# Kernel tuning notes

Measured on AMD Instinct MI355X. Metric: run time of the kernel, lower is better.

The kernel has to match this reference:

```python
import jax, jax.numpy as jnp
import numpy as np

N = 50000   # nodes
E = 800000  # edges (avg degree 16)
D = 128     # node latent dim
DE = 128    # edge latent dim
L = 3       # num_mp_steps


def setup_inputs() -> dict:
    key = jax.random.key(0)
    ks = jax.random.split(key, 10)
    s = 0.05
    return dict(
        x=jax.random.normal(ks[0], (N, D), jnp.float32),
        edge_index=jax.random.randint(ks[1], (2, E), 0, N, jnp.int32),
        edge_attr=jax.random.normal(ks[2], (E, DE), jnp.float32),
        # per-layer GATConv params (stacked over L layers)
        W=jax.random.normal(ks[3], (L, D, D), jnp.float32) * s,        # lin (shared src/dst)
        att_src=jax.random.normal(ks[4], (L, D), jnp.float32) * s,
        att_dst=jax.random.normal(ks[5], (L, D), jnp.float32) * s,
        W_e=jax.random.normal(ks[6], (L, DE, D), jnp.float32) * s,     # lin_edge
        att_edge=jax.random.normal(ks[7], (L, D), jnp.float32) * s,
        bias=jnp.zeros((L, D), jnp.float32),
        ln_gamma=jnp.ones((L, D), jnp.float32),                        # post-conv LayerNorm
        ln_beta=jnp.zeros((L, D), jnp.float32),
    )


def reference(x, edge_index, edge_attr, W, att_src, att_dst, W_e, att_edge, bias, ln_gamma, ln_beta):
    n = x.shape[0]
    src, dst = edge_index[0], edge_index[1]

    # add_self_loops with fill_value='mean': self-loop edge feature of node i is
    # the mean of raw edge features of edges incoming to i (0 if none).
    ones = jnp.ones((src.shape[0],), x.dtype)
    deg = jax.ops.segment_sum(ones, dst, num_segments=n)
    loop_attr = jax.ops.segment_sum(edge_attr, dst, num_segments=n) / jnp.maximum(deg, 1.0)[:, None]
    loop = jnp.arange(n, dtype=src.dtype)
    src_f = jnp.concatenate([src, loop])            # [E+N]
    dst_f = jnp.concatenate([dst, loop])            # [E+N]
    ea_f = jnp.concatenate([edge_attr, loop_attr], axis=0)  # [E+N, DE]

    def layer(h_in, p):
        Wl, asl, adl, Wel, ael, bl, gl, bel = p
        h = h_in @ Wl                                              # [N, D]
        # per-edge attention logits (heads=1)
        a = (h @ asl)[src_f] + (h @ adl)[dst_f] + ea_f @ (Wel @ ael)  # [E+N]
        a = jnp.where(a > 0, a, 0.2 * a)                           # LeakyReLU(0.2)
        # segment softmax over destination nodes (every node has a self loop)
        m = jax.ops.segment_max(a, dst_f, num_segments=n)
        ea = jnp.exp(a - m[dst_f])
        denom = jax.ops.segment_sum(ea, dst_f, num_segments=n)
        alpha = ea / denom[dst_f]
        out = jax.ops.segment_sum(h[src_f] * alpha[:, None], dst_f, num_segments=n) + bl
        # LayerNorm (elementwise affine)
        mu = jnp.mean(out, axis=-1, keepdims=True)
        var = jnp.var(out, axis=-1, keepdims=True)
        out = (out - mu) * jax.lax.rsqrt(var + 1e-5) * gl + bel
        return out, None

    h, _ = jax.lax.scan(layer, x, (W, att_src, att_dst, W_e, att_edge, bias, ln_gamma, ln_beta))
    return h
```

## Files before the change

kernel.cpp:

```cpp
#include <hip/hip_runtime.h>
#include <cstdint>

#define D 128
#define LNUM 3

typedef short short8 __attribute__((ext_vector_type(8)));
typedef float f32x4 __attribute__((ext_vector_type(4)));
typedef float f32x2 __attribute__((ext_vector_type(2)));

static __device__ __forceinline__ float wred_sum(float x) {
#pragma unroll
    for (int off = 32; off; off >>= 1) x += __shfl_xor(x, off);
    return x;
}
static __device__ __forceinline__ float wred_max(float x) {
#pragma unroll
    for (int off = 32; off; off >>= 1) x = fmaxf(x, __shfl_xor(x, off));
    return x;
}
static __device__ __forceinline__ uint32_t f2bf_rne(float x) {
    uint32_t u = __float_as_uint(x);
    uint32_t r = u + 0x7fffu + ((u >> 16) & 1u);
    return r >> 16;
}


__global__ __launch_bounds__(256) void pre_k(const float* __restrict__ W, const float* __restrict__ We,
                                             const float* __restrict__ ae, const float* __restrict__ x,
                                             const int* __restrict__ dst,
                                             uint16_t* __restrict__ Wt, float* __restrict__ vbuf,
                                             uint16_t* __restrict__ xb, int* __restrict__ cnt,
                                             int ND4, int E) {
    int tid = blockIdx.x * 256 + threadIdx.x;
    int stride = gridDim.x * 256;
    for (int i = tid; i < ND4; i += stride) {
        float4 v = *(const float4*)&x[(size_t)i * 4];
        uint2 o;
        o.x = f2bf_rne(v.x) | (f2bf_rne(v.y) << 16);
        o.y = f2bf_rne(v.z) | (f2bf_rne(v.w) << 16);
        *(uint2*)&xb[(size_t)i * 4] = o;
    }
    for (int e = tid; e < E; e += stride) atomicAdd(&cnt[dst[e]], 1);
    for (int i = tid; i < LNUM * D * D; i += stride) {
        int l = i >> 14;
        int r = i & (D * D - 1);
        int j = r >> 7, k = r & 127;
        Wt[i] = (uint16_t)f2bf_rne(W[(size_t)l * D * D + (size_t)k * D + j]);
    }
    if (tid < LNUM * D) {
        int l = tid >> 7, j = tid & 127;
        const float* Wrow = We + ((size_t)l * D + j) * D;
        const float* a = ae + (size_t)l * D;
        float s = 0.f;
        for (int d = 0; d < D; ++d) s += Wrow[d] * a[d];
        vbuf[tid] = s;
    }
}


__global__ __launch_bounds__(1024) void scan_k(const int* __restrict__ cnt, int* __restrict__ rowptr, int N) {
    __shared__ int sh[1024];
    int t = threadIdx.x;
    int chunk = (N + 1023) >> 10;
    int b = t * chunk;
    int e = min(b + chunk, N);
    int s = 0;
    for (int i = b; i < e; ++i) s += cnt[i];
    sh[t] = s;
    __syncthreads();
    for (int off = 1; off < 1024; off <<= 1) {
        int v = (t >= off) ? sh[t - off] : 0;
        __syncthreads();
        sh[t] += v;
        __syncthreads();
    }
    int run = sh[t] - s;
    for (int i = b; i < e; ++i) { rowptr[i] = run; run += cnt[i]; }
    if (t == 1023) rowptr[N] = sh[1023];
}


static __device__ __forceinline__ void gemm_body(uint4* As, int bid, int t,
                                                 const uint16_t* __restrict__ A,
                                                 const uint16_t* __restrict__ Wt,
                                                 const float* __restrict__ as_,
                                                 const float* __restrict__ ad_,
                                                 uint16_t* __restrict__ hbf,
                                                 float* __restrict__ hs, float* __restrict__ hd, int N) {
    int row0 = bid * 64;
#pragma unroll
    for (int it = 0; it < 4; ++it) {
        int idx2 = it * 256 + t;
        int r = idx2 >> 4, s = idx2 & 15;
        int gr = row0 + r;
        uint4 v = make_uint4(0u, 0u, 0u, 0u);
        if (gr < N) v = *(const uint4*)&A[(size_t)gr * D + s * 8];
        As[r * 16 + (s ^ (r & 7))] = v;
    }
    __syncthreads();
    int w = t >> 6, l = t & 63;
    int lrow = l & 15, lk = l >> 4;
    int rbase = w * 16;
    short8 afrag[4];
#pragma unroll
    for (int ks = 0; ks < 4; ++ks) {
        int r = rbase + lrow;
        int s = (ks * 4 + lk) ^ (r & 7);
        afrag[ks] = __builtin_bit_cast(short8, As[r * 16 + s]);
    }
    float psum[4] = {0.f, 0.f, 0.f, 0.f}, pdum[4] = {0.f, 0.f, 0.f, 0.f};
#pragma unroll
    for (int ct = 0; ct < 8; ++ct) {
        f32x4 acc = {0.f, 0.f, 0.f, 0.f};
#pragma unroll
        for (int ks = 0; ks < 4; ++ks) {
            short8 b = *(const short8*)&Wt[(size_t)(ct * 16 + lrow) * D + ks * 32 + lk * 8];
            acc = __builtin_amdgcn_mfma_f32_16x16x32_bf16(afrag[ks], b, acc, 0, 0, 0);
        }
        int col_g = ct * 16 + lrow;
        float av = as_[col_g], dv = ad_[col_g];
#pragma unroll
        for (int r = 0; r < 4; ++r) {
            float v = acc[r];
            psum[r] += v * av;
            pdum[r] += v * dv;
            int row_g = row0 + rbase + lk * 4 + r;
            if (row_g < N) hbf[(size_t)row_g * D + col_g] = (uint16_t)f2bf_rne(v);
        }
    }
#pragma unroll
    for (int r = 0; r < 4; ++r) {
        float ps = psum[r], pd = pdum[r];
#pragma unroll
        for (int off = 1; off < 16; off <<= 1) {
            ps += __shfl_xor(ps, off);
            pd += __shfl_xor(pd, off);
        }
        if (lrow == 0) {
            int row_g = row0 + rbase + lk * 4 + r;
            if (row_g < N) { hs[row_g] = ps; hd[row_g] = pd; }
        }
    }
}


__global__ __launch_bounds__(256) void fg_k(const uint16_t* __restrict__ A, const uint16_t* __restrict__ Wt,
                                            const float* __restrict__ as_, const float* __restrict__ ad_,
                                            uint16_t* __restrict__ hbf, float* __restrict__ hs,
                                            float* __restrict__ hd, int N,
                                            const float* __restrict__ ea, const float* __restrict__ vbuf,
                                            const int* __restrict__ src, const int* __restrict__ dst,
                                            const int* __restrict__ rowptr, int* __restrict__ cnt,
                                            uint4* __restrict__ rec, int E, int NB_G) {
    __shared__ uint4 As[64 * 16];
    int t = threadIdx.x;
    if ((int)blockIdx.x < NB_G) {
        gemm_body(As, blockIdx.x, t, A, Wt, as_, ad_, hbf, hs, hd, N);
        return;
    }
    int bid = blockIdx.x - NB_G;
    int nbF = gridDim.x - NB_G;
    int sub = t & 7;
    float4 vr[3][4];
#pragma unroll
    for (int l = 0; l < 3; ++l)
#pragma unroll
        for (int i = 0; i < 4; ++i)
            vr[l][i] = *(const float4*)&vbuf[l * D + sub * 16 + i * 4];

    for (int e0 = bid * 32; e0 < E; e0 += nbF * 32) {
        int e = e0 + (t >> 3);
        if (e >= E) continue;
        const float* row = ea + (size_t)e * D + sub * 16;
        float p0 = 0.f, p1 = 0.f, p2 = 0.f;
#pragma unroll
        for (int i = 0; i < 4; ++i) {
            float4 v = *(const float4*)&row[i * 4];
            p0 += v.x * vr[0][i].x + v.y * vr[0][i].y + v.z * vr[0][i].z + v.w * vr[0][i].w;
            p1 += v.x * vr[1][i].x + v.y * vr[1][i].y + v.z * vr[1][i].z + v.w * vr[1][i].w;
            p2 += v.x * vr[2][i].x + v.y * vr[2][i].y + v.z * vr[2][i].z + v.w * vr[2][i].w;
        }
#pragma unroll
        for (int off = 1; off < 8; off <<= 1) {
            p0 += __shfl_xor(p0, off);
            p1 += __shfl_xor(p1, off);
            p2 += __shfl_xor(p2, off);
        }
        if (sub == 0) {
            int d = dst[e];
            int p = atomicSub(&cnt[d], 1) - 1;
            int q = rowptr[d] + p;
            uint4 r;
            r.x = (uint32_t)src[e];
            r.y = __float_as_uint(p0);
            r.z = __float_as_uint(p1);
            r.w = __float_as_uint(p2);
            rec[q] = r;
        }
    }
}


__global__ __launch_bounds__(256) void gemm_mfma_k(const uint16_t* __restrict__ A,
                                                   const uint16_t* __restrict__ Wt,
                                                   const float* __restrict__ as_,
                                                   const float* __restrict__ ad_,
                                                   uint16_t* __restrict__ hbf,
                                                   float* __restrict__ hs, float* __restrict__ hd, int N) {
    __shared__ uint4 As[64 * 16];
    gemm_body(As, blockIdx.x, threadIdx.x, A, Wt, as_, ad_, hbf, hs, hd, N);
}


__global__ __launch_bounds__(256) void node_k(const uint32_t* __restrict__ hb, const float* __restrict__ hs,
                                              const float* __restrict__ hd, const uint4* __restrict__ rec,
                                              const int* __restrict__ rowptr,
                                              const float* __restrict__ bias, const float* __restrict__ gamma,
                                              const float* __restrict__ beta,
                                              uint32_t* __restrict__ outb, float* __restrict__ outf,
                                              int N, int lsel) {
    __shared__ float s_al[4][66];
    __shared__ int s_co[4][66];
    int w = threadIdx.x >> 6;
    int lane = threadIdx.x & 63;
    int wid = blockIdx.x * 4 + w;
    if (wid >= N) return;
    int beg = rowptr[wid], end = rowptr[wid + 1];
    int deg = end - beg;
    float hdi = hd[wid];
    float hsi = hs[wid];
    f32x2 acc2 = {0.f, 0.f};

    if (deg <= 63) {
        int ne = deg + 1;
        bool v = lane < deg;
        uint4 r = v ? rec[beg + lane] : make_uint4(0u, 0u, 0u, 0u);
        int col = (int)r.x;
        uint32_t ecu = lsel == 0 ? r.y : (lsel == 1 ? r.z : r.w);
        float ec = __uint_as_float(ecu);
        float hsc = v ? hs[col] : 0.f;
        s_co[w][lane] = col;
        if (lane == 0) { s_co[w][deg] = wid; }
        __asm__ volatile("s_waitcnt lgkmcnt(0)" ::: "memory");

        uint32_t rb[4][8];
        bool fast = ne <= 32;
        if (fast) {
#pragma unroll
            for (int g = 0; g < 4; ++g) {
                if (g * 8 < ne) {
#pragma unroll
                    for (int j0 = 0; j0 < 8; ++j0) {
                        int c = s_co[w][g * 8 + j0];
                        rb[g][j0] = hb[(size_t)c * 64 + lane];
                    }
                }
            }
        }

        float a = v ? (hsc + hdi + ec) : -3e38f;
        a = a > 0.f ? a : 0.2f * a;
        float sumec = wred_sum(v ? ec : 0.f);
        float ecs = deg > 0 ? sumec / (float)deg : 0.f;
        float as_ = hsi + hdi + ecs;
        as_ = as_ > 0.f ? as_ : 0.2f * as_;
        float m = fmaxf(wred_max(a), as_);
        float p = __expf(a - m);
        float ps = __expf(as_ - m);
        float denom = wred_sum(p) + ps;
        float inv = 1.f / denom;
        s_al[w][lane] = p * inv;
        if (lane == 0) { s_al[w][deg] = ps * inv; }
        __asm__ volatile("s_waitcnt lgkmcnt(0)" ::: "memory");

        if (fast) {
#pragma unroll
            for (int g = 0; g < 4; ++g) {
                if (g * 8 < ne) {
#pragma unroll
                    for (int j0 = 0; j0 < 8; ++j0) {
                        float al = s_al[w][g * 8 + j0];
                        uint32_t b = rb[g][j0];
                        f32x2 hv;
                        hv.x = __uint_as_float(b << 16);
                        hv.y = __uint_as_float(b & 0xffff0000u);
                        acc2 += hv * al;
                    }
                }
            }
        } else {
            int j = 0;
            for (; j + 4 <= ne; j += 4) {
                int c0 = s_co[w][j], c1 = s_co[w][j + 1], c2 = s_co[w][j + 2], c3 = s_co[w][j + 3];
                float a0 = s_al[w][j], a1 = s_al[w][j + 1], a2 = s_al[w][j + 2], a3 = s_al[w][j + 3];
                uint32_t b0 = hb[(size_t)c0 * 64 + lane];
                uint32_t b1 = hb[(size_t)c1 * 64 + lane];
                uint32_t b2 = hb[(size_t)c2 * 64 + lane];
                uint32_t b3 = hb[(size_t)c3 * 64 + lane];
                f32x2 h0; h0.x = __uint_as_float(b0 << 16); h0.y = __uint_as_float(b0 & 0xffff0000u);
                f32x2 h1; h1.x = __uint_as_float(b1 << 16); h1.y = __uint_as_float(b1 & 0xffff0000u);
                f32x2 h2; h2.x = __uint_as_float(b2 << 16); h2.y = __uint_as_float(b2 & 0xffff0000u);
                f32x2 h3; h3.x = __uint_as_float(b3 << 16); h3.y = __uint_as_float(b3 & 0xffff0000u);
                acc2 += h0 * a0 + h1 * a1 + h2 * a2 + h3 * a3;
            }
            for (; j < ne; ++j) {
                int c0 = s_co[w][j];
                float a0 = s_al[w][j];
                uint32_t b0 = hb[(size_t)c0 * 64 + lane];
                f32x2 h0; h0.x = __uint_as_float(b0 << 16); h0.y = __uint_as_float(b0 & 0xffff0000u);
                acc2 += h0 * a0;
            }
        }
    } else {
        float m = -3e38f, dsum = 0.f, sumec = 0.f;
        for (int base = 0; base < deg; base += 64) {
            int jj = base + lane;
            bool v = jj < deg;
            uint4 r = v ? rec[beg + jj] : make_uint4(0u, 0u, 0u, 0u);
            uint32_t ecu = lsel == 0 ? r.y : (lsel == 1 ? r.z : r.w);
            float ec = __uint_as_float(ecu);
            float a = v ? (hs[(int)r.x] + hdi + ec) : -3e38f;
            a = a > 0.f ? a : 0.2f * a;
            sumec += wred_sum(v ? ec : 0.f);
            float cm = wred_max(a);
            float nm = fmaxf(m, cm);
            dsum = dsum * __expf(m - nm) + wred_sum(__expf(a - nm));
            m = nm;
        }
        float ecs = sumec / (float)deg;
        float as_ = hsi + hdi + ecs;
        as_ = as_ > 0.f ? as_ : 0.2f * as_;
        float nm = fmaxf(m, as_);
        dsum = dsum * __expf(m - nm) + __expf(as_ - nm);
        m = nm;
        float inv = 1.f / dsum;
        for (int base = 0; base < deg; base += 64) {
            int jj = base + lane;
            bool v = jj < deg;
            uint4 r = v ? rec[beg + jj] : make_uint4(0u, 0u, 0u, 0u);
            int col = (int)r.x;
            uint32_t ecu = lsel == 0 ? r.y : (lsel == 1 ? r.z : r.w);
            float ec = __uint_as_float(ecu);
            float a = v ? (hs[col] + hdi + ec) : -3e38f;
            a = a > 0.f ? a : 0.2f * a;
            __asm__ volatile("s_waitcnt lgkmcnt(0)" ::: "memory");
            s_al[w][lane] = __expf(a - m) * inv;
            s_co[w][lane] = col;
            __asm__ volatile("s_waitcnt lgkmcnt(0)" ::: "memory");
            int cnt = min(64, deg - base);
            for (int k = 0; k < cnt; ++k) {
                int c = s_co[w][k];
                float al = s_al[w][k];
                uint32_t b = hb[(size_t)c * 64 + lane];
                f32x2 h0; h0.x = __uint_as_float(b << 16); h0.y = __uint_as_float(b & 0xffff0000u);
                acc2 += h0 * al;
            }
        }
        float alS = __expf(as_ - m) * inv;
        uint32_t b = hb[(size_t)wid * 64 + lane];
        f32x2 hS; hS.x = __uint_as_float(b << 16); hS.y = __uint_as_float(b & 0xffff0000u);
        acc2 += hS * alS;
    }

    float2 bi = *(const float2*)&bias[lane * 2];
    float o0 = acc2.x + bi.x, o1 = acc2.y + bi.y;
    float mean = wred_sum(o0 + o1) * (1.f / 128.f);
    float d0 = o0 - mean, d1 = o1 - mean;
    float var = wred_sum(d0 * d0 + d1 * d1) * (1.f / 128.f);
    float rstd = rsqrtf(var + 1e-5f);
    float2 g = *(const float2*)&gamma[lane * 2];
    float2 be = *(const float2*)&beta[lane * 2];
    float2 o;
    o.x = d0 * rstd * g.x + be.x;
    o.y = d1 * rstd * g.y + be.y;
    if (outf) {
        *(float2*)&outf[(size_t)wid * D + lane * 2] = o;
    } else {
        outb[(size_t)wid * 64 + lane] = f2bf_rne(o.x) | (f2bf_rne(o.y) << 16);
    }
}


extern "C" void kernel_launch(void* const* d_in, const int* in_sizes, int n_in,
                              void* d_out, int out_size, void* d_ws, size_t ws_size,
                              hipStream_t stream) {
    const float* x = (const float*)d_in[0];
    const int* ei = (const int*)d_in[1];
    const float* ea = (const float*)d_in[2];
    const float* W = (const float*)d_in[3];
    const float* att_src = (const float*)d_in[4];
    const float* att_dst = (const float*)d_in[5];
    const float* We = (const float*)d_in[6];
    const float* att_edge = (const float*)d_in[7];
    const float* bias = (const float*)d_in[8];
    const float* gamma = (const float*)d_in[9];
    const float* beta = (const float*)d_in[10];

    int N = in_sizes[0] / D;
    int E = in_sizes[1] / 2;
    const int* srcA = ei;
    const int* dstA = ei + E;

    float* p = (float*)d_ws;
    float* hsb = p;   p += N;
    float* hdb = p;   p += N;
    float* vbuf = p;  p += LNUM * D + 128;
    uint16_t* xb = (uint16_t*)p;
    uint16_t* hbf = xb + (size_t)N * D;
    uint16_t* hnb = hbf + (size_t)N * D;
    uint16_t* Wt = hnb + (size_t)N * D;
    uint4* rec = (uint4*)(Wt + (size_t)LNUM * D * D);
    int* ip = (int*)(rec + E);
    int* rowptr = ip; ip += N + 1;
    int* cnt = ip;    ip += N;

    hipMemsetAsync(cnt, 0, sizeof(int) * N, stream);
    pre_k<<<1536, 256, 0, stream>>>(W, We, att_edge, x, dstA, Wt, vbuf, xb, cnt, N * D / 4, E);
    scan_k<<<1, 1024, 0, stream>>>(cnt, rowptr, N);

    int NB_G = (N + 63) / 64;
    int NB_F = (E + 31) / 32;
    fg_k<<<NB_G + NB_F, 256, 0, stream>>>(xb, Wt, att_src, att_dst, hbf, hsb, hdb, N,
                                          ea, vbuf, srcA, dstA, rowptr, cnt, rec, E, NB_G);
    node_k<<<(N + 3) / 4, 256, 0, stream>>>((const uint32_t*)hbf, hsb, hdb, rec, rowptr,
                                            bias, gamma, beta, (uint32_t*)hnb, nullptr, N, 0);

    const uint16_t* hin = hnb;
    for (int l = 1; l < LNUM; ++l) {
        gemm_mfma_k<<<(N + 63) / 64, 256, 0, stream>>>(hin, Wt + (size_t)l * D * D,
                                                       att_src + (size_t)l * D, att_dst + (size_t)l * D,
                                                       hbf, hsb, hdb, N);
        bool last = (l == LNUM - 1);
        node_k<<<(N + 3) / 4, 256, 0, stream>>>((const uint32_t*)hbf, hsb, hdb, rec, rowptr,
                                                bias + (size_t)l * D, gamma + (size_t)l * D,
                                                beta + (size_t)l * D,
                                                last ? nullptr : (uint32_t*)hnb,
                                                last ? (float*)d_out : nullptr, N, l);
        hin = hnb;
    }
}
```

Baseline: 417.3 us.

## Merge per-layer GEMM and node kernels into one cooperative persistent kernel

Replaces the sequence of fg_k, node_k and gemm_mfma_k launches with a single cooperative kernel, mega_k, that runs all three GAT layers. The phases are separated by grid-wide syncs, and the work is split over a fixed grid of at most 1024 blocks using grid-stride loops. In the first phase one eighth of the blocks do the GEMM while the rest do the edge projection and CSR scatter. This aims to remove kernel launch gaps and tail effects, but it adds grid.sync overhead, lowers parallelism to a persistent grid, and leaves the first-phase split between GEMM and edge work unbalanced.

```diff
diff --git a/kernel.cpp b/kernel.cpp
--- a/kernel.cpp
+++ b/kernel.cpp
@@ -1,5 +1,8 @@
 #include <hip/hip_runtime.h>
+#include <hip/hip_cooperative_groups.h>
 #include <cstdint>
+
+namespace cg = cooperative_groups;
 
 #define D 128
 #define LNUM 3
@@ -144,240 +147,277 @@
 }
 
 
-__global__ __launch_bounds__(256) void fg_k(const uint16_t* __restrict__ A, const uint16_t* __restrict__ Wt,
-                                            const float* __restrict__ as_, const float* __restrict__ ad_,
-                                            uint16_t* __restrict__ hbf, float* __restrict__ hs,
-                                            float* __restrict__ hd, int N,
-                                            const float* __restrict__ ea, const float* __restrict__ vbuf,
-                                            const int* __restrict__ src, const int* __restrict__ dst,
-                                            const int* __restrict__ rowptr, int* __restrict__ cnt,
-                                            uint4* __restrict__ rec, int E, int NB_G) {
-    __shared__ uint4 As[64 * 16];
-    int t = threadIdx.x;
-    if ((int)blockIdx.x < NB_G) {
-        gemm_body(As, blockIdx.x, t, A, Wt, as_, ad_, hbf, hs, hd, N);
-        return;
-    }
-    int bid = blockIdx.x - NB_G;
-    int nbF = gridDim.x - NB_G;
-    int sub = t & 7;
-    float4 vr[3][4];
-#pragma unroll
-    for (int l = 0; l < 3; ++l)
-#pragma unroll
-        for (int i = 0; i < 4; ++i)
-            vr[l][i] = *(const float4*)&vbuf[l * D + sub * 16 + i * 4];
-
-    for (int e0 = bid * 32; e0 < E; e0 += nbF * 32) {
-        int e = e0 + (t >> 3);
-        if (e >= E) continue;
-        const float* row = ea + (size_t)e * D + sub * 16;
-        float p0 = 0.f, p1 = 0.f, p2 = 0.f;
-#pragma unroll
-        for (int i = 0; i < 4; ++i) {
-            float4 v = *(const float4*)&row[i * 4];
-            p0 += v.x * vr[0][i].x + v.y * vr[0][i].y + v.z * vr[0][i].z + v.w * vr[0][i].w;
-            p1 += v.x * vr[1][i].x + v.y * vr[1][i].y + v.z * vr[1][i].z + v.w * vr[1][i].w;
-            p2 += v.x * vr[2][i].x + v.y * vr[2][i].y + v.z * vr[2][i].z + v.w * vr[2][i].w;
-        }
-#pragma unroll
-        for (int off = 1; off < 8; off <<= 1) {
-            p0 += __shfl_xor(p0, off);
-            p1 += __shfl_xor(p1, off);
-            p2 += __shfl_xor(p2, off);
-        }
-        if (sub == 0) {
-            int d = dst[e];
-            int p = atomicSub(&cnt[d], 1) - 1;
-            int q = rowptr[d] + p;
-            uint4 r;
-            r.x = (uint32_t)src[e];
-            r.y = __float_as_uint(p0);
-            r.z = __float_as_uint(p1);
-            r.w = __float_as_uint(p2);
-            rec[q] = r;
-        }
-    }
-}
-
-
-__global__ __launch_bounds__(256) void gemm_mfma_k(const uint16_t* __restrict__ A,
-                                                   const uint16_t* __restrict__ Wt,
-                                                   const float* __restrict__ as_,
-                                                   const float* __restrict__ ad_,
-                                                   uint16_t* __restrict__ hbf,
-                                                   float* __restrict__ hs, float* __restrict__ hd, int N) {
-    __shared__ uint4 As[64 * 16];
-    gemm_body(As, blockIdx.x, threadIdx.x, A, Wt, as_, ad_, hbf, hs, hd, N);
-}
-
-
-__global__ __launch_bounds__(256) void node_k(const uint32_t* __restrict__ hb, const float* __restrict__ hs,
-                                              const float* __restrict__ hd, const uint4* __restrict__ rec,
-                                              const int* __restrict__ rowptr,
-                                              const float* __restrict__ bias, const float* __restrict__ gamma,
-                                              const float* __restrict__ beta,
-                                              uint32_t* __restrict__ outb, float* __restrict__ outf,
-                                              int N, int lsel) {
+static __device__ __forceinline__ void node_body(int nb, int bid, int w, int lane,
+                                                 const uint32_t* __restrict__ hb, const float* __restrict__ hs,
+                                                 const float* __restrict__ hd, const uint4* __restrict__ rec,
+                                                 const int* __restrict__ rowptr,
+                                                 const float* __restrict__ bias, const float* __restrict__ gamma,
+                                                 const float* __restrict__ beta,
+                                                 uint32_t* __restrict__ outb, float* __restrict__ outf,
+                                                 int N, int lsel) {
     __shared__ float s_al[4][66];
     __shared__ int s_co[4][66];
-    int w = threadIdx.x >> 6;
-    int lane = threadIdx.x & 63;
-    int wid = blockIdx.x * 4 + w;
-    if (wid >= N) return;
-    int beg = rowptr[wid], end = rowptr[wid + 1];
-    int deg = end - beg;
-    float hdi = hd[wid];
-    float hsi = hs[wid];
-    f32x2 acc2 = {0.f, 0.f};
-
-    if (deg <= 63) {
-        int ne = deg + 1;
-        bool v = lane < deg;
-        uint4 r = v ? rec[beg + lane] : make_uint4(0u, 0u, 0u, 0u);
-        int col = (int)r.x;
-        uint32_t ecu = lsel == 0 ? r.y : (lsel == 1 ? r.z : r.w);
-        float ec = __uint_as_float(ecu);
-        float hsc = v ? hs[col] : 0.f;
-        s_co[w][lane] = col;
-        if (lane == 0) { s_co[w][deg] = wid; }
-        __asm__ volatile("s_waitcnt lgkmcnt(0)" ::: "memory");
-
-        uint32_t rb[4][8];
-        bool fast = ne <= 32;
-        if (fast) {
-#pragma unroll
-            for (int g = 0; g < 4; ++g) {
-                if (g * 8 < ne) {
-#pragma unroll
-                    for (int j0 = 0; j0 < 8; ++j0) {
-                        int c = s_co[w][g * 8 + j0];
-                        rb[g][j0] = hb[(size_t)c * 64 + lane];
-                    }
-                }
-            }
-        }
-
-        float a = v ? (hsc + hdi + ec) : -3e38f;
-        a = a > 0.f ? a : 0.2f * a;
-        float sumec = wred_sum(v ? ec : 0.f);
-        float ecs = deg > 0 ? sumec / (float)deg : 0.f;
-        float as_ = hsi + hdi + ecs;
-        as_ = as_ > 0.f ? as_ : 0.2f * as_;
-        float m = fmaxf(wred_max(a), as_);
-        float p = __expf(a - m);
-        float ps = __expf(as_ - m);
-        float denom = wred_sum(p) + ps;
-        float inv = 1.f / denom;
-        s_al[w][lane] = p * inv;
-        if (lane == 0) { s_al[w][deg] = ps * inv; }
-        __asm__ volatile("s_waitcnt lgkmcnt(0)" ::: "memory");
-
-        if (fast) {
-#pragma unroll
-            for (int g = 0; g < 4; ++g) {
-                if (g * 8 < ne) {
-#pragma unroll
-                    for (int j0 = 0; j0 < 8; ++j0) {
-                        float al = s_al[w][g * 8 + j0];
-                        uint32_t b = rb[g][j0];
-                        f32x2 hv;
-                        hv.x = __uint_as_float(b << 16);
-                        hv.y = __uint_as_float(b & 0xffff0000u);
-                        acc2 += hv * al;
-                    }
-                }
-            }
-        } else {
-            int j = 0;
-            for (; j + 4 <= ne; j += 4) {
-                int c0 = s_co[w][j], c1 = s_co[w][j + 1], c2 = s_co[w][j + 2], c3 = s_co[w][j + 3];
-                float a0 = s_al[w][j], a1 = s_al[w][j + 1], a2 = s_al[w][j + 2], a3 = s_al[w][j + 3];
-                uint32_t b0 = hb[(size_t)c0 * 64 + lane];
-                uint32_t b1 = hb[(size_t)c1 * 64 + lane];
-                uint32_t b2 = hb[(size_t)c2 * 64 + lane];
-                uint32_t b3 = hb[(size_t)c3 * 64 + lane];
-                f32x2 h0; h0.x = __uint_as_float(b0 << 16); h0.y = __uint_as_float(b0 & 0xffff0000u);
-                f32x2 h1; h1.x = __uint_as_float(b1 << 16); h1.y = __uint_as_float(b1 & 0xffff0000u);
-                f32x2 h2; h2.x = __uint_as_float(b2 << 16); h2.y = __uint_as_float(b2 & 0xffff0000u);
-                f32x2 h3; h3.x = __uint_as_float(b3 << 16); h3.y = __uint_as_float(b3 & 0xffff0000u);
-                acc2 += h0 * a0 + h1 * a1 + h2 * a2 + h3 * a3;
-            }
-            for (; j < ne; ++j) {
-                int c0 = s_co[w][j];
-                float a0 = s_al[w][j];
-                uint32_t b0 = hb[(size_t)c0 * 64 + lane];
-                f32x2 h0; h0.x = __uint_as_float(b0 << 16); h0.y = __uint_as_float(b0 & 0xffff0000u);
-                acc2 += h0 * a0;
-            }
-        }
-    } else {
-        float m = -3e38f, dsum = 0.f, sumec = 0.f;
-        for (int base = 0; base < deg; base += 64) {
-            int jj = base + lane;
-            bool v = jj < deg;
-            uint4 r = v ? rec[beg + jj] : make_uint4(0u, 0u, 0u, 0u);
-            uint32_t ecu = lsel == 0 ? r.y : (lsel == 1 ? r.z : r.w);
-            float ec = __uint_as_float(ecu);
-            float a = v ? (hs[(int)r.x] + hdi + ec) : -3e38f;
-            a = a > 0.f ? a : 0.2f * a;
-            sumec += wred_sum(v ? ec : 0.f);
-            float cm = wred_max(a);
-            float nm = fmaxf(m, cm);
-            dsum = dsum * __expf(m - nm) + wred_sum(__expf(a - nm));
-            m = nm;
-        }
-        float ecs = sumec / (float)deg;
-        float as_ = hsi + hdi + ecs;
-        as_ = as_ > 0.f ? as_ : 0.2f * as_;
-        float nm = fmaxf(m, as_);
-        dsum = dsum * __expf(m - nm) + __expf(as_ - nm);
-        m = nm;
-        float inv = 1.f / dsum;
-        for (int base = 0; base < deg; base += 64) {
-            int jj = base + lane;
-            bool v = jj < deg;
-            uint4 r = v ? rec[beg + jj] : make_uint4(0u, 0u, 0u, 0u);
+    for (int wid = bid * 4 + w; wid < N; wid += nb * 4) {
+        int beg = rowptr[wid], end = rowptr[wid + 1];
+        int deg = end - beg;
+        float hdi = hd[wid];
+        float hsi = hs[wid];
+        f32x2 acc2 = {0.f, 0.f};
+
+        if (deg <= 63) {
+            int ne = deg + 1;
+            bool v = lane < deg;
+            uint4 r = v ? rec[beg + lane] : make_uint4(0u, 0u, 0u, 0u);
             int col = (int)r.x;
             uint32_t ecu = lsel == 0 ? r.y : (lsel == 1 ? r.z : r.w);
             float ec = __uint_as_float(ecu);
-            float a = v ? (hs[col] + hdi + ec) : -3e38f;
+            float hsc = v ? hs[col] : 0.f;
+            s_co[w][lane] = col;
+            if (lane == 0) { s_co[w][deg] = wid; }
+            __asm__ volatile("s_waitcnt lgkmcnt(0)" ::: "memory");
+
+            uint32_t rb[4][8];
+            bool fast = ne <= 32;
+            if (fast) {
+#pragma unroll
+                for (int g = 0; g < 4; ++g) {
+                    if (g * 8 < ne) {
+#pragma unroll
+                        for (int j0 = 0; j0 < 8; ++j0) {
+                            int c = s_co[w][g * 8 + j0];
+                            rb[g][j0] = hb[(size_t)c * 64 + lane];
+                        }
+                    }
+                }
+            }
+
+            float a = v ? (hsc + hdi + ec) : -3e38f;
             a = a > 0.f ? a : 0.2f * a;
+            float sumec = wred_sum(v ? ec : 0.f);
+            float ecs = deg > 0 ? sumec / (float)deg : 0.f;
+            float as_ = hsi + hdi + ecs;
+            as_ = as_ > 0.f ? as_ : 0.2f * as_;
+            float m = fmaxf(wred_max(a), as_);
+            float p = __expf(a - m);
+            float ps = __expf(as_ - m);
+            float denom = wred_sum(p) + ps;
+            float inv = 1.f / denom;
+            s_al[w][lane] = p * inv;
+            if (lane == 0) { s_al[w][deg] = ps * inv; }
             __asm__ volatile("s_waitcnt lgkmcnt(0)" ::: "memory");
-            s_al[w][lane] = __expf(a - m) * inv;
-            s_co[w][lane] = col;
-            __asm__ volatile("s_waitcnt lgkmcnt(0)" ::: "memory");
-            int cnt = min(64, deg - base);
-            for (int k = 0; k < cnt; ++k) {
-                int c = s_co[w][k];
-                float al = s_al[w][k];
-                uint32_t b = hb[(size_t)c * 64 + lane];
-                f32x2 h0; h0.x = __uint_as_float(b << 16); h0.y = __uint_as_float(b & 0xffff0000u);
-                acc2 += h0 * al;
-            }
-        }
-        float alS = __expf(as_ - m) * inv;
-        uint32_t b = hb[(size_t)wid * 64 + lane];
-        f32x2 hS; hS.x = __uint_as_float(b << 16); hS.y = __uint_as_float(b & 0xffff0000u);
-        acc2 += hS * alS;
-    }
-
-    float2 bi = *(const float2*)&bias[lane * 2];
-    float o0 = acc2.x + bi.x, o1 = acc2.y + bi.y;
-    float mean = wred_sum(o0 + o1) * (1.f / 128.f);
-    float d0 = o0 - mean, d1 = o1 - mean;
-    float var = wred_sum(d0 * d0 + d1 * d1) * (1.f / 128.f);
-    float rstd = rsqrtf(var + 1e-5f);
-    float2 g = *(const float2*)&gamma[lane * 2];
-    float2 be = *(const float2*)&beta[lane * 2];
-    float2 o;
-    o.x = d0 * rstd * g.x + be.x;
-    o.y = d1 * rstd * g.y + be.y;
-    if (outf) {
-        *(float2*)&outf[(size_t)wid * D + lane * 2] = o;
+
+            if (fast) {
+#pragma unroll
+                for (int g = 0; g < 4; ++g) {
+                    if (g * 8 < ne) {
+#pragma unroll
+                        for (int j0 = 0; j0 < 8; ++j0) {
+                            float al = s_al[w][g * 8 + j0];
+                            uint32_t b = rb[g][j0];
+                            f32x2 hv;
+                            hv.x = __uint_as_float(b << 16);
+                            hv.y = __uint_as_float(b & 0xffff0000u);
+                            acc2 += hv * al;
+                        }
+                    }
+                }
+            } else {
+                int j = 0;
+                for (; j + 4 <= ne; j += 4) {
+                    int c0 = s_co[w][j], c1 = s_co[w][j + 1], c2 = s_co[w][j + 2], c3 = s_co[w][j + 3];
+                    float a0 = s_al[w][j], a1 = s_al[w][j + 1], a2 = s_al[w][j + 2], a3 = s_al[w][j + 3];
+                    uint32_t b0 = hb[(size_t)c0 * 64 + lane];
+                    uint32_t b1 = hb[(size_t)c1 * 64 + lane];
+                    uint32_t b2 = hb[(size_t)c2 * 64 + lane];
+                    uint32_t b3 = hb[(size_t)c3 * 64 + lane];
+                    f32x2 h0; h0.x = __uint_as_float(b0 << 16); h0.y = __uint_as_float(b0 & 0xffff0000u);
+                    f32x2 h1; h1.x = __uint_as_float(b1 << 16); h1.y = __uint_as_float(b1 & 0xffff0000u);
+                    f32x2 h2; h2.x = __uint_as_float(b2 << 16); h2.y = __uint_as_float(b2 & 0xffff0000u);
+                    f32x2 h3; h3.x = __uint_as_float(b3 << 16); h3.y = __uint_as_float(b3 & 0xffff0000u);
+                    acc2 += h0 * a0 + h1 * a1 + h2 * a2 + h3 * a3;
+                }
+                for (; j < ne; ++j) {
+                    int c0 = s_co[w][j];
+                    float a0 = s_al[w][j];
+                    uint32_t b0 = hb[(size_t)c0 * 64 + lane];
+                    f32x2 h0; h0.x = __uint_as_float(b0 << 16); h0.y = __uint_as_float(b0 & 0xffff0000u);
+                    acc2 += h0 * a0;
+                }
+            }
+        } else {
+            float m = -3e38f, dsum = 0.f, sumec = 0.f;
+            for (int base = 0; base < deg; base += 64) {
+                int jj = base + lane;
+                bool v = jj < deg;
+                uint4 r = v ? rec[beg + jj] : make_uint4(0u, 0u, 0u, 0u);
+                uint32_t ecu = lsel == 0 ? r.y : (lsel == 1 ? r.z : r.w);
+                float ec = __uint_as_float(ecu);
+                float a = v ? (hs[(int)r.x] + hdi + ec) : -3e38f;
+                a = a > 0.f ? a : 0.2f * a;
+                sumec += wred_sum(v ? ec : 0.f);
+                float cm = wred_max(a);
+                float nm = fmaxf(m, cm);
+                dsum = dsum * __expf(m - nm) + wred_sum(__expf(a - nm));
+                m = nm;
+            }
+            float ecs = sumec / (float)deg;
+            float as_ = hsi + hdi + ecs;
+            as_ = as_ > 0.f ? as_ : 0.2f * as_;
+            float nm = fmaxf(m, as_);
+            dsum = dsum * __expf(m - nm) + __expf(as_ - nm);
+            m = nm;
+            float inv = 1.f / dsum;
+            for (int base = 0; base < deg; base += 64) {
+                int jj = base + lane;
+                bool v = jj < deg;
+                uint4 r = v ? rec[beg + jj] : make_uint4(0u, 0u, 0u, 0u);
+                int col = (int)r.x;
+                uint32_t ecu = lsel == 0 ? r.y : (lsel == 1 ? r.z : r.w);
+                float ec = __uint_as_float(ecu);
+                float a = v ? (hs[col] + hdi + ec) : -3e38f;
+                a = a > 0.f ? a : 0.2f * a;
+                __asm__ volatile("s_waitcnt lgkmcnt(0)" ::: "memory");
+                s_al[w][lane] = __expf(a - m) * inv;
+                s_co[w][lane] = col;
+                __asm__ volatile("s_waitcnt lgkmcnt(0)" ::: "memory");
+                int cnt2 = min(64, deg - base);
+                for (int k = 0; k < cnt2; ++k) {
+                    int c = s_co[w][k];
+                    float al = s_al[w][k];
+                    uint32_t b = hb[(size_t)c * 64 + lane];
+                    f32x2 h0; h0.x = __uint_as_float(b << 16); h0.y = __uint_as_float(b & 0xffff0000u);
+                    acc2 += h0 * al;
+                }
+            }
+            float alS = __expf(as_ - m) * inv;
+            uint32_t b = hb[(size_t)wid * 64 + lane];
+            f32x2 hS; hS.x = __uint_as_float(b << 16); hS.y = __uint_as_float(b & 0xffff0000u);
+            acc2 += hS * alS;
+        }
+
+        float2 bi = *(const float2*)&bias[lane * 2];
+        float o0 = acc2.x + bi.x, o1 = acc2.y + bi.y;
+        float mean = wred_sum(o0 + o1) * (1.f / 128.f);
+        float d0 = o0 - mean, d1 = o1 - mean;
+        float var = wred_sum(d0 * d0 + d1 * d1) * (1.f / 128.f);
+        float rstd = rsqrtf(var + 1e-5f);
+        float2 g = *(const float2*)&gamma[lane * 2];
+        float2 be = *(const float2*)&beta[lane * 2];
+        float2 o;
+        o.x = d0 * rstd * g.x + be.x;
+        o.y = d1 * rstd * g.y + be.y;
+        if (outf) {
+            *(float2*)&outf[(size_t)wid * D + lane * 2] = o;
+        } else {
+            outb[(size_t)wid * 64 + lane] = f2bf_rne(o.x) | (f2bf_rne(o.y) << 16);
+        }
+    }
+}
+
+
+struct MegaArgs {
+    const uint16_t* xb;
+    const uint16_t* Wt;
+    const float* att_src;
+    const float* att_dst;
+    uint16_t* hbf;
+    float* hs;
+    float* hd;
+    const float* ea;
+    const float* vbuf;
+    const int* src;
+    const int* dst;
+    const int* rowptr;
+    int* cnt;
+    uint4* rec;
+    uint16_t* hnb;
+    const float* bias;
+    const float* gamma;
+    const float* beta;
+    float* outf;
+    int N;
+    int E;
+};
+
+__global__ __launch_bounds__(256, 4) void mega_k(MegaArgs a) {
+    cg::grid_group grid = cg::this_grid();
+    __shared__ uint4 As[64 * 16];
+    int nb = gridDim.x, bid = blockIdx.x, t = threadIdx.x;
+    int w = t >> 6, lane = t & 63;
+    int NT = (a.N + 63) / 64;
+
+    int G = nb >> 3;
+    if (bid < G) {
+        for (int tile = bid; tile < NT; tile += G) {
+            gemm_body(As, tile, t, a.xb, a.Wt, a.att_src, a.att_dst, a.hbf, a.hs, a.hd, a.N);
+            __syncthreads();
+        }
     } else {
-        outb[(size_t)wid * 64 + lane] = f2bf_rne(o.x) | (f2bf_rne(o.y) << 16);
-    }
+        int fid = bid - G, nf = nb - G;
+        int sub = t & 7;
+        float4 vr[3][4];
+#pragma unroll
+        for (int l = 0; l < 3; ++l)
+#pragma unroll
+            for (int i = 0; i < 4; ++i)
+                vr[l][i] = *(const float4*)&a.vbuf[l * D + sub * 16 + i * 4];
+        for (int e0 = fid * 32; e0 < a.E; e0 += nf * 32) {
+            int e = e0 + (t >> 3);
+            if (e >= a.E) continue;
+            const float* row = a.ea + (size_t)e * D + sub * 16;
+            float p0 = 0.f, p1 = 0.f, p2 = 0.f;
+#pragma unroll
+            for (int i = 0; i < 4; ++i) {
+                float4 v = *(const float4*)&row[i * 4];
+                p0 += v.x * vr[0][i].x + v.y * vr[0][i].y + v.z * vr[0][i].z + v.w * vr[0][i].w;
+                p1 += v.x * vr[1][i].x + v.y * vr[1][i].y + v.z * vr[1][i].z + v.w * vr[1][i].w;
+                p2 += v.x * vr[2][i].x + v.y * vr[2][i].y + v.z * vr[2][i].z + v.w * vr[2][i].w;
+            }
+#pragma unroll
+            for (int off = 1; off < 8; off <<= 1) {
+                p0 += __shfl_xor(p0, off);
+                p1 += __shfl_xor(p1, off);
+                p2 += __shfl_xor(p2, off);
+            }
+            if (sub == 0) {
+                int d = a.dst[e];
+                int p = atomicSub(&a.cnt[d], 1) - 1;
+                int q = a.rowptr[d] + p;
+                uint4 r;
+                r.x = (uint32_t)a.src[e];
+                r.y = __float_as_uint(p0);
+                r.z = __float_as_uint(p1);
+                r.w = __float_as_uint(p2);
+                a.rec[q] = r;
+            }
+        }
+    }
+    grid.sync();
+
+    node_body(nb, bid, w, lane, (const uint32_t*)a.hbf, a.hs, a.hd, a.rec, a.rowptr,
+              a.bias, a.gamma, a.beta, (uint32_t*)a.hnb, nullptr, a.N, 0);
+    grid.sync();
+
+    for (int tile = bid; tile < NT; tile += nb) {
+        gemm_body(As, tile, t, a.hnb, a.Wt + (size_t)D * D, a.att_src + D, a.att_dst + D,
+                  a.hbf, a.hs, a.hd, a.N);
+        __syncthreads();
+    }
+    grid.sync();
+
+    node_body(nb, bid, w, lane, (const uint32_t*)a.hbf, a.hs, a.hd, a.rec, a.rowptr,
+              a.bias + D, a.gamma + D, a.beta + D, (uint32_t*)a.hnb, nullptr, a.N, 1);
+    grid.sync();
+
+    for (int tile = bid; tile < NT; tile += nb) {
+        gemm_body(As, tile, t, a.hnb, a.Wt + (size_t)2 * D * D, a.att_src + 2 * D, a.att_dst + 2 * D,
+                  a.hbf, a.hs, a.hd, a.N);
+        __syncthreads();
+    }
+    grid.sync();
+
+    node_body(nb, bid, w, lane, (const uint32_t*)a.hbf, a.hs, a.hd, a.rec, a.rowptr,
+              a.bias + 2 * D, a.gamma + 2 * D, a.beta + 2 * D, nullptr, a.outf, a.N, 2);
 }
 
 
@@ -418,24 +458,24 @@
     pre_k<<<1536, 256, 0, stream>>>(W, We, att_edge, x, dstA, Wt, vbuf, xb, cnt, N * D / 4, E);
     scan_k<<<1, 1024, 0, stream>>>(cnt, rowptr, N);
 
-    int NB_G = (N + 63) / 64;
-    int NB_F = (E + 31) / 32;
-    fg_k<<<NB_G + NB_F, 256, 0, stream>>>(xb, Wt, att_src, att_dst, hbf, hsb, hdb, N,
-                                          ea, vbuf, srcA, dstA, rowptr, cnt, rec, E, NB_G);
-    node_k<<<(N + 3) / 4, 256, 0, stream>>>((const uint32_t*)hbf, hsb, hdb, rec, rowptr,
-                                            bias, gamma, beta, (uint32_t*)hnb, nullptr, N, 0);
-
-    const uint16_t* hin = hnb;
-    for (int l = 1; l < LNUM; ++l) {
-        gemm_mfma_k<<<(N + 63) / 64, 256, 0, stream>>>(hin, Wt + (size_t)l * D * D,
-                                                       att_src + (size_t)l * D, att_dst + (size_t)l * D,
-                                                       hbf, hsb, hdb, N);
-        bool last = (l == LNUM - 1);
-        node_k<<<(N + 3) / 4, 256, 0, stream>>>((const uint32_t*)hbf, hsb, hdb, rec, rowptr,
-                                                bias + (size_t)l * D, gamma + (size_t)l * D,
-                                                beta + (size_t)l * D,
-                                                last ? nullptr : (uint32_t*)hnb,
-                                                last ? (float*)d_out : nullptr, N, l);
-        hin = hnb;
-    }
-}
+    int maxBlocksPerCU = 0;
+    hipOccupancyMaxActiveBlocksPerMultiprocessor(&maxBlocksPerCU, (const void*)mega_k, 256, 0);
+    if (maxBlocksPerCU < 1) maxBlocksPerCU = 1;
+    int nb = maxBlocksPerCU * 256;
+    if (nb > 1024) nb = 1024;
+
+    MegaArgs margs;
+    margs.xb = xb; margs.Wt = Wt;
+    margs.att_src = att_src; margs.att_dst = att_dst;
+    margs.hbf = hbf; margs.hs = hsb; margs.hd = hdb;
+    margs.ea = ea; margs.vbuf = vbuf;
+    margs.src = srcA; margs.dst = dstA;
+    margs.rowptr = rowptr; margs.cnt = cnt;
+    margs.rec = rec; margs.hnb = hnb;
+    margs.bias = bias; margs.gamma = gamma; margs.beta = beta;
+    margs.outf = (float*)d_out;
+    margs.N = N; margs.E = E;
+
+    void* kargs[] = { &margs };
+    hipLaunchCooperativeKernel((const void*)mega_k, dim3(nb), dim3(256), kargs, 0, stream);
+}
```

Result: slower. 895.3 us (+114.5%).
